# Optimization experiments

Measured on AMD Instinct MI355X. Metric: run time of the kernel, lower is better.

## Reference

```python
import jax, jax.numpy as jnp
import numpy as np

NEG_INF = -1e18  # fp32 masking constant used by the original module


def setup_inputs() -> dict:
    key0 = jax.random.key(0)
    kq, kk, kv, km, ke = jax.random.split(key0, 5)
    B, L, H, C = 2, 2048, 16, 64
    query = jax.random.normal(kq, (B, L, H, C), dtype=jnp.float32)
    key = jax.random.normal(kk, (B, L, H, C), dtype=jnp.float32)
    value = jax.random.normal(kv, (B, L, H, C), dtype=jnp.float32)
    mask = jax.random.randint(km, (B, L, L), 0, 2).astype(jnp.bool_)
    edge_scores = jax.random.normal(ke, (1, H, L, L), dtype=jnp.float32)
    return {"query": query, "key": key, "value": value, "mask": mask,
            "edge_scores": edge_scores}


def _masked_softmax(att_score, mask):
    # mask: True -> keep, False -> masked. Fill with -1e18 (fp32 path),
    # softmax, then multiply by mask (post-softmax zeroing), as in original.
    s = jnp.where(mask, att_score, NEG_INF)
    w = jax.nn.softmax(s, axis=-1)
    return w * mask.astype(w.dtype)


def reference(query, key, value, mask, edge_scores):
    # layout 'NTK': query/key/value (B, L, H, C); mask (B, Lq, Lm)
    scale = jnp.sqrt(jnp.asarray(query.shape[-1], dtype=query.dtype))
    # scores: (B, H, Lq, Lm)
    scores = jnp.einsum('binc,bjnc->bnij', query, key)
    scores = scores + edge_scores
    attn_weights = _masked_softmax(scores / scale, mask[:, None, :, :])
    # dropout rate is 0.0 -> identity
    # context: (B, Lq, H, Cv) -> (B, Lq, H*Cv)
    context = jnp.einsum('bnij,bjnc->binc', attn_weights, value)
    B, Lq = context.shape[0], context.shape[1]
    context_vec = context.reshape(B, Lq, -1)
    return (context_vec, scores, attn_weights)
```

## Files before the change

### kernel.cpp

```cpp
#include <hip/hip_runtime.h>


typedef __attribute__((ext_vector_type(8))) short bf16x8;
typedef __attribute__((ext_vector_type(4))) float f32x4;
typedef __attribute__((ext_vector_type(4))) int   i32x4;

#define LQ 2048
#define NH 16
#define CD 64

__device__ inline short f2bf(float x) {
    union { float f; unsigned u; } v; v.f = x;
    unsigned r = v.u + 0x7FFFu + ((v.u >> 16) & 1u);
    return (short)(r >> 16);
}

__device__ inline bf16x8 pack8(f32x4 a, f32x4 b) {
    bf16x8 r;
    r[0] = f2bf(a[0]); r[1] = f2bf(a[1]); r[2] = f2bf(a[2]); r[3] = f2bf(a[3]);
    r[4] = f2bf(b[0]); r[5] = f2bf(b[1]); r[6] = f2bf(b[2]); r[7] = f2bf(b[3]);
    return r;
}

__device__ inline void lds_barrier() {
    asm volatile("s_waitcnt lgkmcnt(0)" ::: "memory");
    __builtin_amdgcn_s_barrier();
}

__global__ __launch_bounds__(256, 4)
void k_main(const float* __restrict__ q, const float* __restrict__ kk,
            const float* __restrict__ v, const int* __restrict__ mask,
            const float* __restrict__ edge,
            float* __restrict__ sc, float* __restrict__ attn,
            float* __restrict__ ctx, float* __restrict__ invout)
{
    __shared__ short Ks[64][66];
    __shared__ short Vt[64][66];
    __shared__ short Wt[4][16][66];

    const int flat = blockIdx.x;
    const int L = (flat & 7) * 128 + (flat >> 3);
    const int z = L >> 5;
    const int i0 = (L & 31) * 64;
    const int b = z & 1, h = z >> 1;

    const int tid = threadIdx.x;
    const int r = tid >> 2, seg = (tid & 3) * 16;
    const int wave = tid >> 6, lane = tid & 63;
    const int quad = lane >> 4, mm = lane & 15;

    const int gi = i0 + wave * 16 + mm;
    const float* qp = q + ((size_t)((b * LQ + gi) * NH + h)) * CD;
    bf16x8 qa0 = pack8(*(const f32x4*)(qp + quad * 8), *(const f32x4*)(qp + quad * 8 + 4));
    bf16x8 qa1 = pack8(*(const f32x4*)(qp + 32 + quad * 8), *(const f32x4*)(qp + 32 + quad * 8 + 4));

    const float* erow = edge + ((size_t)(h * LQ + gi)) * LQ;
    const int*   mrow = mask + ((size_t)(b * LQ + gi)) * LQ;
    const size_t srow = ((size_t)((b * NH + h) * LQ + gi)) * LQ;

    f32x4 ev[4]; i32x4 mv[4];
    #pragma unroll
    for (int jt = 0; jt < 4; ++jt) {
        ev[jt] = *(const f32x4*)(erow + jt * 16 + quad * 4);
        mv[jt] = *(const i32x4*)(mrow + jt * 16 + quad * 4);
    }
    f32x4 kr[4], vr[4];
    {
        const float* kp = kk + ((size_t)((b * LQ + r) * NH + h)) * CD + seg;
        const float* vp = v  + ((size_t)((b * LQ + r) * NH + h)) * CD + seg;
        #pragma unroll
        for (int u = 0; u < 4; ++u) { kr[u] = ((const f32x4*)kp)[u]; vr[u] = ((const f32x4*)vp)[u]; }
    }

    float lacc = 0.f;
    f32x4 cacc[4] = { {0,0,0,0}, {0,0,0,0}, {0,0,0,0}, {0,0,0,0} };

    for (int jb = 0; jb < 32; ++jb) {
        const int j0 = jb * 64;
        #pragma unroll
        for (int u = 0; u < 4; ++u) {
            *(short4*)&Ks[r][seg + u * 4] =
                make_short4(f2bf(kr[u][0]), f2bf(kr[u][1]), f2bf(kr[u][2]), f2bf(kr[u][3]));
            Vt[seg + u * 4 + 0][r] = f2bf(vr[u][0]);
            Vt[seg + u * 4 + 1][r] = f2bf(vr[u][1]);
            Vt[seg + u * 4 + 2][r] = f2bf(vr[u][2]);
            Vt[seg + u * 4 + 3][r] = f2bf(vr[u][3]);
        }
        lds_barrier();

        f32x4 acc[4];
        #pragma unroll
        for (int jt = 0; jt < 4; ++jt) {
            bf16x8 k0 = *(const bf16x8*)&Ks[jt * 16 + mm][quad * 8];
            bf16x8 k1 = *(const bf16x8*)&Ks[jt * 16 + mm][32 + quad * 8];
            f32x4 a = {0.f, 0.f, 0.f, 0.f};
            a = __builtin_amdgcn_mfma_f32_16x16x32_bf16(k0, qa0, a, 0, 0, 0);
            a = __builtin_amdgcn_mfma_f32_16x16x32_bf16(k1, qa1, a, 0, 0, 0);
            acc[jt] = a;
        }

        if (jb < 31) {
            const float* kp = kk + ((size_t)((b * LQ + j0 + 64 + r) * NH + h)) * CD + seg;
            const float* vp = v  + ((size_t)((b * LQ + j0 + 64 + r) * NH + h)) * CD + seg;
            #pragma unroll
            for (int u = 0; u < 4; ++u) { kr[u] = ((const f32x4*)kp)[u]; vr[u] = ((const f32x4*)vp)[u]; }
        }

        #pragma unroll
        for (int jt = 0; jt < 4; ++jt) {
            const int jl = jt * 16 + quad * 4;
            f32x4 s4 = acc[jt] + ev[jt];
            *(f32x4*)(sc + srow + j0 + jl) = s4;
            f32x4 p;
            p[0] = mv[jt][0] ? __expf(s4[0] * 0.125f) : 0.f;
            p[1] = mv[jt][1] ? __expf(s4[1] * 0.125f) : 0.f;
            p[2] = mv[jt][2] ? __expf(s4[2] * 0.125f) : 0.f;
            p[3] = mv[jt][3] ? __expf(s4[3] * 0.125f) : 0.f;
            *(f32x4*)(attn + srow + j0 + jl) = p;
            *(short4*)&Wt[wave][mm][jl] = make_short4(f2bf(p[0]), f2bf(p[1]), f2bf(p[2]), f2bf(p[3]));
            lacc += (p[0] + p[1]) + (p[2] + p[3]);
        }

        if (jb < 31) {
            #pragma unroll
            for (int jt = 0; jt < 4; ++jt) {
                ev[jt] = *(const f32x4*)(erow + j0 + 64 + jt * 16 + quad * 4);
                mv[jt] = *(const i32x4*)(mrow + j0 + 64 + jt * 16 + quad * 4);
            }
        }

        #pragma unroll
        for (int kt = 0; kt < 2; ++kt) {
            bf16x8 aw = *(const bf16x8*)&Wt[wave][mm][kt * 32 + quad * 8];
            #pragma unroll
            for (int nt = 0; nt < 4; ++nt) {
                bf16x8 bb = *(const bf16x8*)&Vt[nt * 16 + mm][kt * 32 + quad * 8];
                cacc[nt] = __builtin_amdgcn_mfma_f32_16x16x32_bf16(aw, bb, cacc[nt], 0, 0, 0);
            }
        }
        lds_barrier();
    }

    lacc += __shfl_xor(lacc, 16, 64);
    lacc += __shfl_xor(lacc, 32, 64);
    const float inv = (lacc > 0.f) ? 1.f / lacc : 0.f;
    if (quad == 0)
        invout[(size_t)(b * NH + h) * LQ + gi] = inv;

    float inv4[4];
    #pragma unroll
    for (int reg = 0; reg < 4; ++reg)
        inv4[reg] = __shfl(inv, quad * 4 + reg, 64);

    const int irow = i0 + wave * 16 + quad * 4;
    #pragma unroll
    for (int nt = 0; nt < 4; ++nt) {
        const int c = nt * 16 + mm;
        #pragma unroll
        for (int reg = 0; reg < 4; ++reg) {
            const int i = irow + reg;
            ctx[((size_t)(b * LQ + i)) * (NH * CD) + h * CD + c] = cacc[nt][reg] * inv4[reg];
        }
    }
}

__global__ __launch_bounds__(256)
void k_norm(float* __restrict__ attn, const float* __restrict__ inv)
{
    const size_t total4 = (size_t)2 * NH * LQ * LQ / 4;
    size_t idx = (size_t)blockIdx.x * 256 + threadIdx.x;
    const size_t stride = (size_t)gridDim.x * 256;
    for (; idx < total4; idx += stride) {
        const float iv = inv[(idx * 4) >> 11];
        f32x4 w = __builtin_nontemporal_load((const f32x4*)attn + idx);
        w *= iv;
        __builtin_nontemporal_store(w, (f32x4*)attn + idx);
    }
}

extern "C" void kernel_launch(void* const* d_in, const int* in_sizes, int n_in,
                              void* d_out, int out_size, void* d_ws, size_t ws_size,
                              hipStream_t stream) {
    const float* q    = (const float*)d_in[0];
    const float* k    = (const float*)d_in[1];
    const float* v    = (const float*)d_in[2];
    const int*   mask = (const int*)d_in[3];
    const float* edge = (const float*)d_in[4];

    float* out = (float*)d_out;
    float* ctx = out;
    float* sc  = out + 4194304;
    float* at  = sc + 134217728;

    float* inv = (float*)d_ws;

    k_main<<<dim3(1024), 256, 0, stream>>>(q, k, v, mask, edge, sc, at, ctx, inv);
    k_norm<<<dim3(2048), 256, 0, stream>>>(at, inv);
}
```

Before: 1.684 ms.

## Transpose score tile through LDS for row-contiguous global score/attn stores

```diff
diff --git a/kernel.cpp b/kernel.cpp
--- a/kernel.cpp
+++ b/kernel.cpp
@@ -26,6 +26,9 @@
     asm volatile("s_waitcnt lgkmcnt(0)" ::: "memory");
     __builtin_amdgcn_s_barrier();
 }
+
+#define SF_IDX(w,r,c) ((((w)*16+(r))*68) + (c))
+#define WT_IDX(w,r,c) ((((w)*16+(r))*136) + (c))
 
 __global__ __launch_bounds__(256, 4)
 void k_main(const float* __restrict__ q, const float* __restrict__ kk,
@@ -34,9 +37,11 @@
             float* __restrict__ sc, float* __restrict__ attn,
             float* __restrict__ ctx, float* __restrict__ invout)
 {
-    __shared__ short Ks[64][66];
-    __shared__ short Vt[64][66];
-    __shared__ short Wt[4][16][66];
+    __shared__ short Ks[64][72];
+    __shared__ short Vt[64][72];
+    __shared__ __align__(16) char SfW[4 * 16 * 68 * 4];
+    float* SFp = (float*)SfW;
+    short* WTp = (short*)SfW;
 
     const int flat = blockIdx.x;
     const int L = (flat & 7) * 128 + (flat >> 3);
@@ -49,20 +54,17 @@
     const int wave = tid >> 6, lane = tid & 63;
     const int quad = lane >> 4, mm = lane & 15;
 
-    const int gi = i0 + wave * 16 + mm;
-    const float* qp = q + ((size_t)((b * LQ + gi) * NH + h)) * CD;
+    const int gq = i0 + wave * 16 + mm;
+    const float* qp = q + ((size_t)((b * LQ + gq) * NH + h)) * CD;
     bf16x8 qa0 = pack8(*(const f32x4*)(qp + quad * 8), *(const f32x4*)(qp + quad * 8 + 4));
     bf16x8 qa1 = pack8(*(const f32x4*)(qp + 32 + quad * 8), *(const f32x4*)(qp + 32 + quad * 8 + 4));
 
-    const float* erow = edge + ((size_t)(h * LQ + gi)) * LQ;
-    const int*   mrow = mask + ((size_t)(b * LQ + gi)) * LQ;
-    const size_t srow = ((size_t)((b * NH + h) * LQ + gi)) * LQ;
-
     f32x4 ev[4]; i32x4 mv[4];
     #pragma unroll
-    for (int jt = 0; jt < 4; ++jt) {
-        ev[jt] = *(const f32x4*)(erow + jt * 16 + quad * 4);
-        mv[jt] = *(const i32x4*)(mrow + jt * 16 + quad * 4);
+    for (int s = 0; s < 4; ++s) {
+        const int gi = i0 + wave * 16 + quad + 4 * s;
+        ev[s] = *(const f32x4*)(edge + ((size_t)(h * LQ + gi)) * LQ + mm * 4);
+        mv[s] = *(const i32x4*)(mask + ((size_t)(b * LQ + gi)) * LQ + mm * 4);
     }
     f32x4 kr[4], vr[4];
     {
@@ -72,7 +74,7 @@
         for (int u = 0; u < 4; ++u) { kr[u] = ((const f32x4*)kp)[u]; vr[u] = ((const f32x4*)vp)[u]; }
     }
 
-    float lacc = 0.f;
+    float lacc[4] = {0.f, 0.f, 0.f, 0.f};
     f32x4 cacc[4] = { {0,0,0,0}, {0,0,0,0}, {0,0,0,0}, {0,0,0,0} };
 
     for (int jb = 0; jb < 32; ++jb) {
@@ -107,31 +109,40 @@
         }
 
         #pragma unroll
-        for (int jt = 0; jt < 4; ++jt) {
-            const int jl = jt * 16 + quad * 4;
-            f32x4 s4 = acc[jt] + ev[jt];
-            *(f32x4*)(sc + srow + j0 + jl) = s4;
+        for (int jt = 0; jt < 4; ++jt)
+            *(f32x4*)&SFp[SF_IDX(wave, mm, jt * 16 + quad * 4)] = acc[jt];
+
+        #pragma unroll
+        for (int s = 0; s < 4; ++s) {
+            const int rl = quad + 4 * s;
+            const int gi = i0 + wave * 16 + rl;
+            f32x4 sv = *(const f32x4*)&SFp[SF_IDX(wave, rl, mm * 4)];
+            f32x4 s4 = sv + ev[s];
+            const size_t sidx = ((size_t)((b * NH + h) * LQ + gi)) * LQ + j0 + mm * 4;
+            *(f32x4*)(sc + sidx) = s4;
             f32x4 p;
-            p[0] = mv[jt][0] ? __expf(s4[0] * 0.125f) : 0.f;
-            p[1] = mv[jt][1] ? __expf(s4[1] * 0.125f) : 0.f;
-            p[2] = mv[jt][2] ? __expf(s4[2] * 0.125f) : 0.f;
-            p[3] = mv[jt][3] ? __expf(s4[3] * 0.125f) : 0.f;
-            *(f32x4*)(attn + srow + j0 + jl) = p;
-            *(short4*)&Wt[wave][mm][jl] = make_short4(f2bf(p[0]), f2bf(p[1]), f2bf(p[2]), f2bf(p[3]));
-            lacc += (p[0] + p[1]) + (p[2] + p[3]);
+            p[0] = mv[s][0] ? __expf(s4[0] * 0.125f) : 0.f;
+            p[1] = mv[s][1] ? __expf(s4[1] * 0.125f) : 0.f;
+            p[2] = mv[s][2] ? __expf(s4[2] * 0.125f) : 0.f;
+            p[3] = mv[s][3] ? __expf(s4[3] * 0.125f) : 0.f;
+            *(f32x4*)(attn + sidx) = p;
+            *(short4*)&WTp[WT_IDX(wave, rl, mm * 4)] =
+                make_short4(f2bf(p[0]), f2bf(p[1]), f2bf(p[2]), f2bf(p[3]));
+            lacc[s] += (p[0] + p[1]) + (p[2] + p[3]);
         }
 
         if (jb < 31) {
             #pragma unroll
-            for (int jt = 0; jt < 4; ++jt) {
-                ev[jt] = *(const f32x4*)(erow + j0 + 64 + jt * 16 + quad * 4);
-                mv[jt] = *(const i32x4*)(mrow + j0 + 64 + jt * 16 + quad * 4);
+            for (int s = 0; s < 4; ++s) {
+                const int gi = i0 + wave * 16 + quad + 4 * s;
+                ev[s] = *(const f32x4*)(edge + ((size_t)(h * LQ + gi)) * LQ + j0 + 64 + mm * 4);
+                mv[s] = *(const i32x4*)(mask + ((size_t)(b * LQ + gi)) * LQ + j0 + 64 + mm * 4);
             }
         }
 
         #pragma unroll
         for (int kt = 0; kt < 2; ++kt) {
-            bf16x8 aw = *(const bf16x8*)&Wt[wave][mm][kt * 32 + quad * 8];
+            bf16x8 aw = *(const bf16x8*)&WTp[WT_IDX(wave, mm, kt * 32 + quad * 8)];
             #pragma unroll
             for (int nt = 0; nt < 4; ++nt) {
                 bf16x8 bb = *(const bf16x8*)&Vt[nt * 16 + mm][kt * 32 + quad * 8];
@@ -141,16 +152,26 @@
         lds_barrier();
     }
 
-    lacc += __shfl_xor(lacc, 16, 64);
-    lacc += __shfl_xor(lacc, 32, 64);
-    const float inv = (lacc > 0.f) ? 1.f / lacc : 0.f;
-    if (quad == 0)
-        invout[(size_t)(b * NH + h) * LQ + gi] = inv;
-
+    float inv_s[4];
+    #pragma unroll
+    for (int s = 0; s < 4; ++s) {
+        float t = lacc[s];
+        #pragma unroll
+        for (int o = 1; o <= 8; o <<= 1) t += __shfl_xor(t, o, 64);
+        inv_s[s] = (t > 0.f) ? 1.f / t : 0.f;
+        if (mm == 0)
+            invout[(size_t)(b * NH + h) * LQ + i0 + wave * 16 + quad + 4 * s] = inv_s[s];
+    }
+
+    if (mm == 0) {
+        #pragma unroll
+        for (int s = 0; s < 4; ++s)
+            SFp[SF_IDX(wave, 0, quad + 4 * s)] = inv_s[s];
+    }
     float inv4[4];
     #pragma unroll
     for (int reg = 0; reg < 4; ++reg)
-        inv4[reg] = __shfl(inv, quad * 4 + reg, 64);
+        inv4[reg] = SFp[SF_IDX(wave, 0, quad * 4 + reg)];
 
     const int irow = i0 + wave * 16 + quad * 4;
     #pragma unroll
```

After: 1.776 ms. 5.5% more time.

## Compute softmax row sums in a first pass, drop separate normalization kernel

Applied to the files above, without the earlier changes.

```diff
diff --git a/kernel.cpp b/kernel.cpp
--- a/kernel.cpp
+++ b/kernel.cpp
@@ -28,13 +28,13 @@
 }
 
 __global__ __launch_bounds__(256, 4)
-void k_main(const float* __restrict__ q, const float* __restrict__ kk,
+void k_attn(const float* __restrict__ q, const float* __restrict__ kk,
             const float* __restrict__ v, const int* __restrict__ mask,
             const float* __restrict__ edge,
             float* __restrict__ sc, float* __restrict__ attn,
-            float* __restrict__ ctx, float* __restrict__ invout)
+            float* __restrict__ ctx)
 {
-    __shared__ short Ks[64][66];
+    __shared__ short KsD[2][64][66];
     __shared__ short Vt[64][66];
     __shared__ short Wt[4][16][66];
 
@@ -58,28 +58,91 @@
     const int*   mrow = mask + ((size_t)(b * LQ + gi)) * LQ;
     const size_t srow = ((size_t)((b * NH + h) * LQ + gi)) * LQ;
 
+    const float* kbase = kk + ((size_t)((b * LQ + r) * NH + h)) * CD + seg;
+    const float* vbase = v  + ((size_t)((b * LQ + r) * NH + h)) * CD + seg;
+    const size_t kstep = (size_t)64 * NH * CD;
+
     f32x4 ev[4]; i32x4 mv[4];
     #pragma unroll
     for (int jt = 0; jt < 4; ++jt) {
         ev[jt] = *(const f32x4*)(erow + jt * 16 + quad * 4);
         mv[jt] = *(const i32x4*)(mrow + jt * 16 + quad * 4);
     }
-    f32x4 kr[4], vr[4];
-    {
-        const float* kp = kk + ((size_t)((b * LQ + r) * NH + h)) * CD + seg;
-        const float* vp = v  + ((size_t)((b * LQ + r) * NH + h)) * CD + seg;
-        #pragma unroll
-        for (int u = 0; u < 4; ++u) { kr[u] = ((const f32x4*)kp)[u]; vr[u] = ((const f32x4*)vp)[u]; }
-    }
+
+    f32x4 kr[4];
+    #pragma unroll
+    for (int u = 0; u < 4; ++u) kr[u] = ((const f32x4*)kbase)[u];
+    #pragma unroll
+    for (int u = 0; u < 4; ++u)
+        *(short4*)&KsD[0][r][seg + u * 4] =
+            make_short4(f2bf(kr[u][0]), f2bf(kr[u][1]), f2bf(kr[u][2]), f2bf(kr[u][3]));
+    #pragma unroll
+    for (int u = 0; u < 4; ++u) kr[u] = ((const f32x4*)(kbase + kstep))[u];
+    lds_barrier();
 
     float lacc = 0.f;
-    f32x4 cacc[4] = { {0,0,0,0}, {0,0,0,0}, {0,0,0,0}, {0,0,0,0} };
-
     for (int jb = 0; jb < 32; ++jb) {
         const int j0 = jb * 64;
+        const int cur = jb & 1;
+        if (jb < 31) {
+            #pragma unroll
+            for (int u = 0; u < 4; ++u)
+                *(short4*)&KsD[cur ^ 1][r][seg + u * 4] =
+                    make_short4(f2bf(kr[u][0]), f2bf(kr[u][1]), f2bf(kr[u][2]), f2bf(kr[u][3]));
+            if (jb < 30) {
+                const float* kp = kbase + kstep * (jb + 2);
+                #pragma unroll
+                for (int u = 0; u < 4; ++u) kr[u] = ((const f32x4*)kp)[u];
+            }
+        }
+        f32x4 acc[4];
+        #pragma unroll
+        for (int jt = 0; jt < 4; ++jt) {
+            bf16x8 k0 = *(const bf16x8*)&KsD[cur][jt * 16 + mm][quad * 8];
+            bf16x8 k1 = *(const bf16x8*)&KsD[cur][jt * 16 + mm][32 + quad * 8];
+            f32x4 a = {0.f, 0.f, 0.f, 0.f};
+            a = __builtin_amdgcn_mfma_f32_16x16x32_bf16(k0, qa0, a, 0, 0, 0);
+            a = __builtin_amdgcn_mfma_f32_16x16x32_bf16(k1, qa1, a, 0, 0, 0);
+            acc[jt] = a;
+        }
+        #pragma unroll
+        for (int jt = 0; jt < 4; ++jt) {
+            f32x4 s4 = acc[jt] + ev[jt];
+            *(f32x4*)(sc + srow + j0 + jt * 16 + quad * 4) = s4;
+            lacc += (mv[jt][0] ? __expf(s4[0] * 0.125f) : 0.f)
+                  + (mv[jt][1] ? __expf(s4[1] * 0.125f) : 0.f)
+                  + (mv[jt][2] ? __expf(s4[2] * 0.125f) : 0.f)
+                  + (mv[jt][3] ? __expf(s4[3] * 0.125f) : 0.f);
+        }
+        if (jb < 31) {
+            #pragma unroll
+            for (int jt = 0; jt < 4; ++jt) {
+                ev[jt] = *(const f32x4*)(erow + j0 + 64 + jt * 16 + quad * 4);
+                mv[jt] = *(const i32x4*)(mrow + j0 + 64 + jt * 16 + quad * 4);
+            }
+        }
+        lds_barrier();
+    }
+
+    lacc += __shfl_xor(lacc, 16, 64);
+    lacc += __shfl_xor(lacc, 32, 64);
+    const float inv = (lacc > 0.f) ? 1.f / lacc : 0.f;
+
+    f32x4 vr[4];
+    #pragma unroll
+    for (int u = 0; u < 4; ++u) { kr[u] = ((const f32x4*)kbase)[u]; vr[u] = ((const f32x4*)vbase)[u]; }
+    #pragma unroll
+    for (int jt = 0; jt < 4; ++jt) {
+        ev[jt] = *(const f32x4*)(erow + jt * 16 + quad * 4);
+        mv[jt] = *(const i32x4*)(mrow + jt * 16 + quad * 4);
+    }
+    f32x4 cacc[4] = { {0,0,0,0}, {0,0,0,0}, {0,0,0,0}, {0,0,0,0} };
+
+    for (int jb = 0; jb < 32; ++jb) {
+        const int j0 = jb * 64;
         #pragma unroll
         for (int u = 0; u < 4; ++u) {
-            *(short4*)&Ks[r][seg + u * 4] =
+            *(short4*)&KsD[0][r][seg + u * 4] =
                 make_short4(f2bf(kr[u][0]), f2bf(kr[u][1]), f2bf(kr[u][2]), f2bf(kr[u][3]));
             Vt[seg + u * 4 + 0][r] = f2bf(vr[u][0]);
             Vt[seg + u * 4 + 1][r] = f2bf(vr[u][1]);
@@ -91,8 +154,8 @@
         f32x4 acc[4];
         #pragma unroll
         for (int jt = 0; jt < 4; ++jt) {
-            bf16x8 k0 = *(const bf16x8*)&Ks[jt * 16 + mm][quad * 8];
-            bf16x8 k1 = *(const bf16x8*)&Ks[jt * 16 + mm][32 + quad * 8];
+            bf16x8 k0 = *(const bf16x8*)&KsD[0][jt * 16 + mm][quad * 8];
+            bf16x8 k1 = *(const bf16x8*)&KsD[0][jt * 16 + mm][32 + quad * 8];
             f32x4 a = {0.f, 0.f, 0.f, 0.f};
             a = __builtin_amdgcn_mfma_f32_16x16x32_bf16(k0, qa0, a, 0, 0, 0);
             a = __builtin_amdgcn_mfma_f32_16x16x32_bf16(k1, qa1, a, 0, 0, 0);
@@ -100,8 +163,8 @@
         }
 
         if (jb < 31) {
-            const float* kp = kk + ((size_t)((b * LQ + j0 + 64 + r) * NH + h)) * CD + seg;
-            const float* vp = v  + ((size_t)((b * LQ + j0 + 64 + r) * NH + h)) * CD + seg;
+            const float* kp = kbase + kstep * (jb + 1);
+            const float* vp = vbase + kstep * (jb + 1);
             #pragma unroll
             for (int u = 0; u < 4; ++u) { kr[u] = ((const f32x4*)kp)[u]; vr[u] = ((const f32x4*)vp)[u]; }
         }
@@ -110,15 +173,13 @@
         for (int jt = 0; jt < 4; ++jt) {
             const int jl = jt * 16 + quad * 4;
             f32x4 s4 = acc[jt] + ev[jt];
-            *(f32x4*)(sc + srow + j0 + jl) = s4;
-            f32x4 p;
-            p[0] = mv[jt][0] ? __expf(s4[0] * 0.125f) : 0.f;
-            p[1] = mv[jt][1] ? __expf(s4[1] * 0.125f) : 0.f;
-            p[2] = mv[jt][2] ? __expf(s4[2] * 0.125f) : 0.f;
-            p[3] = mv[jt][3] ? __expf(s4[3] * 0.125f) : 0.f;
-            *(f32x4*)(attn + srow + j0 + jl) = p;
-            *(short4*)&Wt[wave][mm][jl] = make_short4(f2bf(p[0]), f2bf(p[1]), f2bf(p[2]), f2bf(p[3]));
-            lacc += (p[0] + p[1]) + (p[2] + p[3]);
+            f32x4 w;
+            w[0] = mv[jt][0] ? __expf(s4[0] * 0.125f) * inv : 0.f;
+            w[1] = mv[jt][1] ? __expf(s4[1] * 0.125f) * inv : 0.f;
+            w[2] = mv[jt][2] ? __expf(s4[2] * 0.125f) * inv : 0.f;
+            w[3] = mv[jt][3] ? __expf(s4[3] * 0.125f) * inv : 0.f;
+            *(f32x4*)(attn + srow + j0 + jl) = w;
+            *(short4*)&Wt[wave][mm][jl] = make_short4(f2bf(w[0]), f2bf(w[1]), f2bf(w[2]), f2bf(w[3]));
         }
 
         if (jb < 31) {
@@ -141,17 +202,6 @@
         lds_barrier();
     }
 
-    lacc += __shfl_xor(lacc, 16, 64);
-    lacc += __shfl_xor(lacc, 32, 64);
-    const float inv = (lacc > 0.f) ? 1.f / lacc : 0.f;
-    if (quad == 0)
-        invout[(size_t)(b * NH + h) * LQ + gi] = inv;
-
-    float inv4[4];
-    #pragma unroll
-    for (int reg = 0; reg < 4; ++reg)
-        inv4[reg] = __shfl(inv, quad * 4 + reg, 64);
-
     const int irow = i0 + wave * 16 + quad * 4;
     #pragma unroll
     for (int nt = 0; nt < 4; ++nt) {
@@ -159,22 +209,8 @@
         #pragma unroll
         for (int reg = 0; reg < 4; ++reg) {
             const int i = irow + reg;
-            ctx[((size_t)(b * LQ + i)) * (NH * CD) + h * CD + c] = cacc[nt][reg] * inv4[reg];
-        }
-    }
-}
-
-__global__ __launch_bounds__(256)
-void k_norm(float* __restrict__ attn, const float* __restrict__ inv)
-{
-    const size_t total4 = (size_t)2 * NH * LQ * LQ / 4;
-    size_t idx = (size_t)blockIdx.x * 256 + threadIdx.x;
-    const size_t stride = (size_t)gridDim.x * 256;
-    for (; idx < total4; idx += stride) {
-        const float iv = inv[(idx * 4) >> 11];
-        f32x4 w = __builtin_nontemporal_load((const f32x4*)attn + idx);
-        w *= iv;
-        __builtin_nontemporal_store(w, (f32x4*)attn + idx);
+            ctx[((size_t)(b * LQ + i)) * (NH * CD) + h * CD + c] = cacc[nt][reg];
+        }
     }
 }
 
@@ -192,8 +228,5 @@
     float* sc  = out + 4194304;
     float* at  = sc + 134217728;
 
-    float* inv = (float*)d_ws;
-
-    k_main<<<dim3(1024), 256, 0, stream>>>(q, k, v, mask, edge, sc, at, ctx, inv);
-    k_norm<<<dim3(2048), 256, 0, stream>>>(at, inv);
-}
+    k_attn<<<dim3(1024), 256, 0, stream>>>(q, k, v, mask, edge, sc, at, ctx);
+}
```

Result: faster. 1.646 ms (-2.2%).

## Split attention into score pass and normalized weight pass, drop separate normalization kernel

Applied to the files above, without the earlier changes.

```diff
diff --git a/kernel.cpp b/kernel.cpp
--- a/kernel.cpp
+++ b/kernel.cpp
@@ -8,6 +8,7 @@
 #define LQ 2048
 #define NH 16
 #define CD 64
+#define NHC (NH*CD)
 
 __device__ inline short f2bf(float x) {
     union { float f; unsigned u; } v; v.f = x;
@@ -22,22 +23,42 @@
     return r;
 }
 
-__device__ inline void lds_barrier() {
-    asm volatile("s_waitcnt lgkmcnt(0)" ::: "memory");
-    __builtin_amdgcn_s_barrier();
+__global__ __launch_bounds__(256)
+void k_prep(const float* __restrict__ kk, const float* __restrict__ v,
+            short* __restrict__ Kb, short* __restrict__ Vt)
+{
+    const int bz = blockIdx.x >> 5;
+    const int j0 = (blockIdx.x & 31) * 64;
+    const int b = bz & 1, h = bz >> 1;
+    const int tid = threadIdx.x;
+
+    const int r = tid >> 2, seg = (tid & 3) * 16;
+    const size_t kidx = ((size_t)((b * LQ + j0 + r) * NH + h)) * CD + seg;
+    #pragma unroll
+    for (int u = 0; u < 4; ++u) {
+        f32x4 g = *(const f32x4*)(kk + kidx + u * 4);
+        *(short4*)(Kb + kidx + u * 4) =
+            make_short4(f2bf(g[0]), f2bf(g[1]), f2bf(g[2]), f2bf(g[3]));
+    }
+
+    const int rgrp = tid >> 4, c4 = tid & 15;
+    const float* vp = v + ((size_t)((b * LQ + j0 + rgrp * 4) * NH + h)) * CD + c4 * 4;
+    f32x4 va0 = *(const f32x4*)vp;
+    f32x4 va1 = *(const f32x4*)(vp + NHC);
+    f32x4 va2 = *(const f32x4*)(vp + 2 * NHC);
+    f32x4 va3 = *(const f32x4*)(vp + 3 * NHC);
+    #pragma unroll
+    for (int cs = 0; cs < 4; ++cs) {
+        *(short4*)(Vt + ((size_t)((b * NH + h) * CD + c4 * 4 + cs)) * LQ + j0 + rgrp * 4) =
+            make_short4(f2bf(va0[cs]), f2bf(va1[cs]), f2bf(va2[cs]), f2bf(va3[cs]));
+    }
 }
 
 __global__ __launch_bounds__(256, 4)
-void k_main(const float* __restrict__ q, const float* __restrict__ kk,
-            const float* __restrict__ v, const int* __restrict__ mask,
-            const float* __restrict__ edge,
-            float* __restrict__ sc, float* __restrict__ attn,
-            float* __restrict__ ctx, float* __restrict__ invout)
+void k_A(const float* __restrict__ q, const short* __restrict__ Kb,
+         const float* __restrict__ edge, const int* __restrict__ mask,
+         float* __restrict__ sc, float* __restrict__ invout)
 {
-    __shared__ short Ks[64][66];
-    __shared__ short Vt[64][66];
-    __shared__ short Wt[4][16][66];
-
     const int flat = blockIdx.x;
     const int L = (flat & 7) * 128 + (flat >> 3);
     const int z = L >> 5;
@@ -45,11 +66,10 @@
     const int b = z & 1, h = z >> 1;
 
     const int tid = threadIdx.x;
-    const int r = tid >> 2, seg = (tid & 3) * 16;
     const int wave = tid >> 6, lane = tid & 63;
     const int quad = lane >> 4, mm = lane & 15;
-
     const int gi = i0 + wave * 16 + mm;
+
     const float* qp = q + ((size_t)((b * LQ + gi) * NH + h)) * CD;
     bf16x8 qa0 = pack8(*(const f32x4*)(qp + quad * 8), *(const f32x4*)(qp + quad * 8 + 4));
     bf16x8 qa1 = pack8(*(const f32x4*)(qp + 32 + quad * 8), *(const f32x4*)(qp + 32 + quad * 8 + 4));
@@ -57,6 +77,7 @@
     const float* erow = edge + ((size_t)(h * LQ + gi)) * LQ;
     const int*   mrow = mask + ((size_t)(b * LQ + gi)) * LQ;
     const size_t srow = ((size_t)((b * NH + h) * LQ + gi)) * LQ;
+    const short* kfb = Kb + (size_t)b * LQ * NHC + (size_t)h * CD;
 
     f32x4 ev[4]; i32x4 mv[4];
     #pragma unroll
@@ -64,63 +85,30 @@
         ev[jt] = *(const f32x4*)(erow + jt * 16 + quad * 4);
         mv[jt] = *(const i32x4*)(mrow + jt * 16 + quad * 4);
     }
-    f32x4 kr[4], vr[4];
-    {
-        const float* kp = kk + ((size_t)((b * LQ + r) * NH + h)) * CD + seg;
-        const float* vp = v  + ((size_t)((b * LQ + r) * NH + h)) * CD + seg;
-        #pragma unroll
-        for (int u = 0; u < 4; ++u) { kr[u] = ((const f32x4*)kp)[u]; vr[u] = ((const f32x4*)vp)[u]; }
-    }
 
     float lacc = 0.f;
-    f32x4 cacc[4] = { {0,0,0,0}, {0,0,0,0}, {0,0,0,0}, {0,0,0,0} };
-
     for (int jb = 0; jb < 32; ++jb) {
         const int j0 = jb * 64;
-        #pragma unroll
-        for (int u = 0; u < 4; ++u) {
-            *(short4*)&Ks[r][seg + u * 4] =
-                make_short4(f2bf(kr[u][0]), f2bf(kr[u][1]), f2bf(kr[u][2]), f2bf(kr[u][3]));
-            Vt[seg + u * 4 + 0][r] = f2bf(vr[u][0]);
-            Vt[seg + u * 4 + 1][r] = f2bf(vr[u][1]);
-            Vt[seg + u * 4 + 2][r] = f2bf(vr[u][2]);
-            Vt[seg + u * 4 + 3][r] = f2bf(vr[u][3]);
-        }
-        lds_barrier();
-
         f32x4 acc[4];
         #pragma unroll
         for (int jt = 0; jt < 4; ++jt) {
-            bf16x8 k0 = *(const bf16x8*)&Ks[jt * 16 + mm][quad * 8];
-            bf16x8 k1 = *(const bf16x8*)&Ks[jt * 16 + mm][32 + quad * 8];
+            const short* kr = kfb + (size_t)(j0 + jt * 16 + mm) * NHC + quad * 8;
+            bf16x8 k0 = *(const bf16x8*)kr;
+            bf16x8 k1 = *(const bf16x8*)(kr + 32);
             f32x4 a = {0.f, 0.f, 0.f, 0.f};
             a = __builtin_amdgcn_mfma_f32_16x16x32_bf16(k0, qa0, a, 0, 0, 0);
             a = __builtin_amdgcn_mfma_f32_16x16x32_bf16(k1, qa1, a, 0, 0, 0);
             acc[jt] = a;
         }
-
-        if (jb < 31) {
-            const float* kp = kk + ((size_t)((b * LQ + j0 + 64 + r) * NH + h)) * CD + seg;
-            const float* vp = v  + ((size_t)((b * LQ + j0 + 64 + r) * NH + h)) * CD + seg;
-            #pragma unroll
-            for (int u = 0; u < 4; ++u) { kr[u] = ((const f32x4*)kp)[u]; vr[u] = ((const f32x4*)vp)[u]; }
-        }
-
         #pragma unroll
         for (int jt = 0; jt < 4; ++jt) {
-            const int jl = jt * 16 + quad * 4;
             f32x4 s4 = acc[jt] + ev[jt];
-            *(f32x4*)(sc + srow + j0 + jl) = s4;
-            f32x4 p;
-            p[0] = mv[jt][0] ? __expf(s4[0] * 0.125f) : 0.f;
-            p[1] = mv[jt][1] ? __expf(s4[1] * 0.125f) : 0.f;
-            p[2] = mv[jt][2] ? __expf(s4[2] * 0.125f) : 0.f;
-            p[3] = mv[jt][3] ? __expf(s4[3] * 0.125f) : 0.f;
-            *(f32x4*)(attn + srow + j0 + jl) = p;
-            *(short4*)&Wt[wave][mm][jl] = make_short4(f2bf(p[0]), f2bf(p[1]), f2bf(p[2]), f2bf(p[3]));
-            lacc += (p[0] + p[1]) + (p[2] + p[3]);
-        }
-
+            *(f32x4*)(sc + srow + j0 + jt * 16 + quad * 4) = s4;
+            lacc += (mv[jt][0] ? __expf(s4[0] * 0.125f) : 0.f)
+                  + (mv[jt][1] ? __expf(s4[1] * 0.125f) : 0.f)
+                  + (mv[jt][2] ? __expf(s4[2] * 0.125f) : 0.f)
+                  + (mv[jt][3] ? __expf(s4[3] * 0.125f) : 0.f);
+        }
         if (jb < 31) {
             #pragma unroll
             for (int jt = 0; jt < 4; ++jt) {
@@ -128,29 +116,93 @@
                 mv[jt] = *(const i32x4*)(mrow + j0 + 64 + jt * 16 + quad * 4);
             }
         }
-
-        #pragma unroll
-        for (int kt = 0; kt < 2; ++kt) {
-            bf16x8 aw = *(const bf16x8*)&Wt[wave][mm][kt * 32 + quad * 8];
-            #pragma unroll
-            for (int nt = 0; nt < 4; ++nt) {
-                bf16x8 bb = *(const bf16x8*)&Vt[nt * 16 + mm][kt * 32 + quad * 8];
-                cacc[nt] = __builtin_amdgcn_mfma_f32_16x16x32_bf16(aw, bb, cacc[nt], 0, 0, 0);
-            }
-        }
-        lds_barrier();
     }
 
     lacc += __shfl_xor(lacc, 16, 64);
     lacc += __shfl_xor(lacc, 32, 64);
-    const float inv = (lacc > 0.f) ? 1.f / lacc : 0.f;
     if (quad == 0)
-        invout[(size_t)(b * NH + h) * LQ + gi] = inv;
-
-    float inv4[4];
-    #pragma unroll
-    for (int reg = 0; reg < 4; ++reg)
-        inv4[reg] = __shfl(inv, quad * 4 + reg, 64);
+        invout[(size_t)(b * NH + h) * LQ + gi] = (lacc > 0.f) ? 1.f / lacc : 0.f;
+}
+
+__global__ __launch_bounds__(256, 4)
+void k_B(const short* __restrict__ Vt, const int* __restrict__ mask,
+         const float* __restrict__ invws, const float* __restrict__ sc,
+         float* __restrict__ attn, float* __restrict__ ctx)
+{
+    const int flat = blockIdx.x;
+    const int L = (flat & 7) * 128 + (flat >> 3);
+    const int z = L >> 5;
+    const int i0 = (L & 31) * 64;
+    const int b = z & 1, h = z >> 1;
+
+    const int tid = threadIdx.x;
+    const int wave = tid >> 6, lane = tid & 63;
+    const int quad = lane >> 4, mm = lane & 15;
+    const int gi = i0 + wave * 16 + mm;
+
+    const int*   mrow = mask + ((size_t)(b * LQ + gi)) * LQ;
+    const size_t srow = ((size_t)((b * NH + h) * LQ + gi)) * LQ;
+    const float  inv  = invws[(size_t)(b * NH + h) * LQ + gi];
+    const short* vtb  = Vt + (size_t)(b * NH + h) * CD * LQ;
+
+    f32x4 s0a = *(const f32x4*)(sc + srow + quad * 8);
+    f32x4 s0b = *(const f32x4*)(sc + srow + quad * 8 + 4);
+    f32x4 s1a = *(const f32x4*)(sc + srow + 32 + quad * 8);
+    f32x4 s1b = *(const f32x4*)(sc + srow + 32 + quad * 8 + 4);
+    i32x4 m0a = *(const i32x4*)(mrow + quad * 8);
+    i32x4 m0b = *(const i32x4*)(mrow + quad * 8 + 4);
+    i32x4 m1a = *(const i32x4*)(mrow + 32 + quad * 8);
+    i32x4 m1b = *(const i32x4*)(mrow + 32 + quad * 8 + 4);
+
+    f32x4 cacc[4] = { {0,0,0,0}, {0,0,0,0}, {0,0,0,0}, {0,0,0,0} };
+
+    for (int jb = 0; jb < 32; ++jb) {
+        const int j0 = jb * 64;
+        f32x4 wa, wb2;
+        wa[0] = m0a[0] ? __expf(s0a[0] * 0.125f) * inv : 0.f;
+        wa[1] = m0a[1] ? __expf(s0a[1] * 0.125f) * inv : 0.f;
+        wa[2] = m0a[2] ? __expf(s0a[2] * 0.125f) * inv : 0.f;
+        wa[3] = m0a[3] ? __expf(s0a[3] * 0.125f) * inv : 0.f;
+        wb2[0] = m0b[0] ? __expf(s0b[0] * 0.125f) * inv : 0.f;
+        wb2[1] = m0b[1] ? __expf(s0b[1] * 0.125f) * inv : 0.f;
+        wb2[2] = m0b[2] ? __expf(s0b[2] * 0.125f) * inv : 0.f;
+        wb2[3] = m0b[3] ? __expf(s0b[3] * 0.125f) * inv : 0.f;
+        *(f32x4*)(attn + srow + j0 + quad * 8) = wa;
+        *(f32x4*)(attn + srow + j0 + quad * 8 + 4) = wb2;
+        bf16x8 aw0 = pack8(wa, wb2);
+        wa[0] = m1a[0] ? __expf(s1a[0] * 0.125f) * inv : 0.f;
+        wa[1] = m1a[1] ? __expf(s1a[1] * 0.125f) * inv : 0.f;
+        wa[2] = m1a[2] ? __expf(s1a[2] * 0.125f) * inv : 0.f;
+        wa[3] = m1a[3] ? __expf(s1a[3] * 0.125f) * inv : 0.f;
+        wb2[0] = m1b[0] ? __expf(s1b[0] * 0.125f) * inv : 0.f;
+        wb2[1] = m1b[1] ? __expf(s1b[1] * 0.125f) * inv : 0.f;
+        wb2[2] = m1b[2] ? __expf(s1b[2] * 0.125f) * inv : 0.f;
+        wb2[3] = m1b[3] ? __expf(s1b[3] * 0.125f) * inv : 0.f;
+        *(f32x4*)(attn + srow + j0 + 32 + quad * 8) = wa;
+        *(f32x4*)(attn + srow + j0 + 32 + quad * 8 + 4) = wb2;
+        bf16x8 aw1 = pack8(wa, wb2);
+
+        if (jb < 31) {
+            const int jn = j0 + 64;
+            s0a = *(const f32x4*)(sc + srow + jn + quad * 8);
+            s0b = *(const f32x4*)(sc + srow + jn + quad * 8 + 4);
+            s1a = *(const f32x4*)(sc + srow + jn + 32 + quad * 8);
+            s1b = *(const f32x4*)(sc + srow + jn + 32 + quad * 8 + 4);
+            m0a = *(const i32x4*)(mrow + jn + quad * 8);
+            m0b = *(const i32x4*)(mrow + jn + quad * 8 + 4);
+            m1a = *(const i32x4*)(mrow + jn + 32 + quad * 8);
+            m1b = *(const i32x4*)(mrow + jn + 32 + quad * 8 + 4);
+        }
+
+        #pragma unroll
+        for (int nt = 0; nt < 4; ++nt) {
+            const short* vr = vtb + (size_t)(nt * 16 + mm) * LQ + j0 + quad * 8;
+            bf16x8 b0 = *(const bf16x8*)vr;
+            bf16x8 b1 = *(const bf16x8*)(vr + 32);
+            cacc[nt] = __builtin_amdgcn_mfma_f32_16x16x32_bf16(aw0, b0, cacc[nt], 0, 0, 0);
+            cacc[nt] = __builtin_amdgcn_mfma_f32_16x16x32_bf16(aw1, b1, cacc[nt], 0, 0, 0);
+        }
+    }
 
     const int irow = i0 + wave * 16 + quad * 4;
     #pragma unroll
@@ -159,22 +211,8 @@
         #pragma unroll
         for (int reg = 0; reg < 4; ++reg) {
             const int i = irow + reg;
-            ctx[((size_t)(b * LQ + i)) * (NH * CD) + h * CD + c] = cacc[nt][reg] * inv4[reg];
-        }
-    }
-}
-
-__global__ __launch_bounds__(256)
-void k_norm(float* __restrict__ attn, const float* __restrict__ inv)
-{
-    const size_t total4 = (size_t)2 * NH * LQ * LQ / 4;
-    size_t idx = (size_t)blockIdx.x * 256 + threadIdx.x;
-    const size_t stride = (size_t)gridDim.x * 256;
-    for (; idx < total4; idx += stride) {
-        const float iv = inv[(idx * 4) >> 11];
-        f32x4 w = __builtin_nontemporal_load((const f32x4*)attn + idx);
-        w *= iv;
-        __builtin_nontemporal_store(w, (f32x4*)attn + idx);
+            ctx[((size_t)(b * LQ + i)) * NHC + h * CD + c] = cacc[nt][reg];
+        }
     }
 }
 
@@ -192,8 +230,11 @@
     float* sc  = out + 4194304;
     float* at  = sc + 134217728;
 
-    float* inv = (float*)d_ws;
-
-    k_main<<<dim3(1024), 256, 0, stream>>>(q, k, v, mask, edge, sc, at, ctx, inv);
-    k_norm<<<dim3(2048), 256, 0, stream>>>(at, inv);
-}
+    short* Kb  = (short*)d_ws;
+    short* Vt  = (short*)d_ws + 4194304;
+    float* inv = (float*)((char*)d_ws + 16777216);
+
+    k_prep<<<dim3(1024), 256, 0, stream>>>(k, v, Kb, Vt);
+    k_A   <<<dim3(1024), 256, 0, stream>>>(q, Kb, edge, mask, sc, inv);
+    k_B   <<<dim3(1024), 256, 0, stream>>>(Vt, mask, inv, sc, at, ctx);
+}
```

After: 1.765 ms. +4.8%, slower.
